# Performance work log

Hardware: AMD Instinct MI355X
Metric: run time of the kernel (lower is better)

## Reference

```python
import jax, jax.numpy as jnp
import numpy as np

N_NODES = 50000
N_EDGES = 800000
IN_CH = 128
H = [128, 128, 128]


def _sage_max(x, src, dst, Wl, b, Wr, n_nodes):
    # PyG SAGEConv(aggr='max'): max-aggregate neighbor features, then
    # out = agg @ Wl.T + b + x @ Wr.T ; empty segments -> 0 (torch_scatter).
    agg = jax.ops.segment_max(x[src], dst, num_segments=n_nodes)  # [N, d]
    agg = jnp.where(jnp.isfinite(agg), agg, 0.0)
    return agg @ Wl.T + b + x @ Wr.T


def setup_inputs() -> dict:
    key = jax.random.key(0)
    ks = jax.random.split(key, 24)
    x = jax.random.normal(ks[0], (N_NODES, IN_CH), dtype=jnp.float32)
    edge_index = jax.random.randint(ks[1], (2, N_EDGES), 0, N_NODES, dtype=jnp.int64)
    s = 0.05

    def w(k, o, i):
        return jax.random.normal(k, (o, i), dtype=jnp.float32) * s

    inp = {
        "x": x,
        "edge_index": edge_index,
        "shared_Wl": w(ks[2], H[0], IN_CH), "shared_b": jnp.zeros((H[0],), jnp.float32), "shared_Wr": w(ks[3], H[0], IN_CH),
        "rt1_Wl": w(ks[4], H[1], H[0]), "rt1_b": jnp.zeros((H[1],), jnp.float32), "rt1_Wr": w(ks[5], H[1], H[0]),
        "rt2_Wl": w(ks[6], H[2], H[1]), "rt2_b": jnp.zeros((H[2],), jnp.float32), "rt2_Wr": w(ks[7], H[2], H[1]),
        "rt3_W": w(ks[8], 1, H[2]), "rt3_b": jnp.zeros((1,), jnp.float32),
        "mv1_Wl": w(ks[9], H[1], H[0]), "mv1_b": jnp.zeros((H[1],), jnp.float32), "mv1_Wr": w(ks[10], H[1], H[0]),
        "mv2_Wl": w(ks[11], H[2], H[1]), "mv2_b": jnp.zeros((H[2],), jnp.float32), "mv2_Wr": w(ks[12], H[2], H[1]),
        "mv3_W": w(ks[13], 1, H[2]), "mv3_b": jnp.zeros((1,), jnp.float32),
    }
    return inp


def reference(x, edge_index, shared_Wl, shared_b, shared_Wr,
              rt1_Wl, rt1_b, rt1_Wr, rt2_Wl, rt2_b, rt2_Wr, rt3_W, rt3_b,
              mv1_Wl, mv1_b, mv1_Wr, mv2_Wl, mv2_b, mv2_Wr, mv3_W, mv3_b):
    n = x.shape[0]
    src, dst = edge_index[0], edge_index[1]
    # Eval mode: dropout is identity.
    mv = jax.nn.relu(_sage_max(x, src, dst, shared_Wl, shared_b, shared_Wr, n))

    rt = jax.nn.relu(_sage_max(mv, src, dst, rt1_Wl, rt1_b, rt1_Wr, n))
    rt = jax.nn.relu(_sage_max(rt, src, dst, rt2_Wl, rt2_b, rt2_Wr, n))
    rtAngle = (rt @ rt3_W.T + rt3_b).reshape(-1)

    md = jax.nn.relu(_sage_max(mv, src, dst, mv1_Wl, mv1_b, mv1_Wr, n))
    md = jax.nn.relu(_sage_max(md, src, dst, mv2_Wl, mv2_b, mv2_Wr, n))
    moveDis = (md @ mv3_W.T + mv3_b).reshape(-1)

    return (rtAngle, moveDis)
```

## Files before the change

kernel.cpp:

```cpp
#include <hip/hip_runtime.h>
#include <hip/hip_bf16.h>
#include <math.h>

#define NN 50000
#define NE 800000
#define C  128
#define NR 8
#define RNG (NN / NR)
typedef unsigned int u32;
typedef unsigned short u16;

using f32x4  = __attribute__((ext_vector_type(4))) float;
using short8 = __attribute__((ext_vector_type(8))) short;

__device__ __forceinline__ u16 f2bf(float f) {
    u32 u = __float_as_uint(f);
    u32 r = u + 0x7FFFu + ((u >> 16) & 1u);
    return (u16)(r >> 16);
}
__device__ __forceinline__ float bf2f(u16 h) {
    return __uint_as_float(((u32)h) << 16);
}

__device__ __forceinline__ void gload_lds16(const u16* g, u16* l) {
    __builtin_amdgcn_global_load_lds(
        (const __attribute__((address_space(1))) u32*)g,
        (__attribute__((address_space(3))) u32*)l,
        16, 0, 0);
}


__global__ void k_zero(int* __restrict__ p, int n) {
    int i = blockIdx.x * blockDim.x + threadIdx.x;
    if (i < n) p[i] = 0;
}

__global__ __launch_bounds__(256) void k_hist_x(const int* __restrict__ dst, int* __restrict__ deg, int nE) {
    int r    = blockIdx.x & (NR - 1);
    int base = (blockIdx.x >> 3) * 4096;
    int lo   = r * RNG, hi = lo + RNG;
    #pragma unroll
    for (int it = 0; it < 16; ++it) {
        int e = base + it * 256 + threadIdx.x;
        if (e < nE) {
            int d = dst[e];
            if (d >= lo && d < hi) atomicAdd(&deg[d], 1);
        }
    }
}

__global__ __launch_bounds__(1024) void k_scan_blk(const int* __restrict__ deg, int* __restrict__ rowptr,
                                                   int* __restrict__ bsum, int n) {
    __shared__ int wsum[16];
    int tid = threadIdx.x, lane = tid & 63, wid = tid >> 6;
    int i = blockIdx.x * 1024 + tid;
    int v = (i < n) ? deg[i] : 0;
    int incl = v;
    #pragma unroll
    for (int d = 1; d < 64; d <<= 1) {
        int t = __shfl_up(incl, d, 64);
        if (lane >= d) incl += t;
    }
    if (lane == 63) wsum[wid] = incl;
    __syncthreads();
    int wo = 0;
    #pragma unroll
    for (int w = 0; w < 16; ++w) wo += (w < wid) ? wsum[w] : 0;
    if (i < n) rowptr[i + 1] = wo + incl;
    if (tid == 1023) bsum[blockIdx.x] = wo + incl;
}

__global__ void k_scan_sums(int* __restrict__ bsum, int nb) {
    int lane = threadIdx.x;
    int v = (lane < nb) ? bsum[lane] : 0;
    int incl = v;
    #pragma unroll
    for (int d = 1; d < 64; d <<= 1) {
        int t = __shfl_up(incl, d, 64);
        if (lane >= d) incl += t;
    }
    if (lane < nb) bsum[lane] = incl - v;
}

__global__ __launch_bounds__(1024) void k_scan_add(int* __restrict__ rowptr, const int* __restrict__ bsum, int n) {
    int i = blockIdx.x * 1024 + threadIdx.x;
    if (i == 0) rowptr[0] = 0;
    if (i < n) rowptr[i + 1] += bsum[blockIdx.x];
}

__global__ __launch_bounds__(256) void k_fill_x(const int* __restrict__ src, const int* __restrict__ dst,
                                                const int* __restrict__ rowptr, int* __restrict__ deg,
                                                u16* __restrict__ esrc, int nE) {
    int r    = blockIdx.x & (NR - 1);
    int base = (blockIdx.x >> 3) * 4096;
    int lo   = r * RNG, hi = lo + RNG;
    #pragma unroll
    for (int it = 0; it < 16; ++it) {
        int e = base + it * 256 + threadIdx.x;
        if (e < nE) {
            int d = dst[e];
            if (d >= lo && d < hi) {
                int old = atomicSub(&deg[d], 1);
                esrc[rowptr[d + 1] - old] = (u16)src[e];
            }
        }
    }
}

__global__ void k_cvt(const float* __restrict__ in, u32* __restrict__ oh, int n64) {
    int i = blockIdx.x * 256 + threadIdx.x;
    if (i < n64) {
        float2 v = *(const float2*)(in + (size_t)i * 2);
        oh[i] = ((u32)f2bf(v.x)) | (((u32)f2bf(v.y)) << 16);
    }
}

#define UPK(w_, lo_, hi_) { lo_ = fmaxf(lo_, __uint_as_float((w_) << 16)); \
                            hi_ = fmaxf(hi_, __uint_as_float((w_) & 0xFFFF0000u)); }

__global__ __launch_bounds__(256) void k_segmax_bf(const u32* __restrict__ h2, const int* __restrict__ rowptr,
                                                   const u16* __restrict__ esrc, u32* __restrict__ agg2, int n) {
    int node = blockIdx.x * 4 + (threadIdx.x >> 6);
    int lane = threadIdx.x & 63;
    if (node >= n) return;
    int beg = rowptr[node], end = rowptr[node + 1];
    float mlo = -INFINITY, mhi = -INFINITY;
    int last = end - 1;
    for (int i = beg; i < end; i += 8) {
        int e0 = i,     e1 = i + 1, e2 = i + 2, e3 = i + 3;
        int e4 = i + 4, e5 = i + 5, e6 = i + 6, e7 = i + 7;
        e1 = e1 > last ? last : e1;  e2 = e2 > last ? last : e2;
        e3 = e3 > last ? last : e3;  e4 = e4 > last ? last : e4;
        e5 = e5 > last ? last : e5;  e6 = e6 > last ? last : e6;
        e7 = e7 > last ? last : e7;
        u32 w0 = h2[((size_t)esrc[e0] << 6) + lane];
        u32 w1 = h2[((size_t)esrc[e1] << 6) + lane];
        u32 w2 = h2[((size_t)esrc[e2] << 6) + lane];
        u32 w3 = h2[((size_t)esrc[e3] << 6) + lane];
        u32 w4 = h2[((size_t)esrc[e4] << 6) + lane];
        u32 w5 = h2[((size_t)esrc[e5] << 6) + lane];
        u32 w6 = h2[((size_t)esrc[e6] << 6) + lane];
        u32 w7 = h2[((size_t)esrc[e7] << 6) + lane];
        UPK(w0, mlo, mhi) UPK(w1, mlo, mhi) UPK(w2, mlo, mhi) UPK(w3, mlo, mhi)
        UPK(w4, mlo, mhi) UPK(w5, mlo, mhi) UPK(w6, mlo, mhi) UPK(w7, mlo, mhi)
    }
    u32 r = 0u;
    if (end > beg)
        r = (__float_as_uint(mlo) >> 16) | (__float_as_uint(mhi) & 0xFFFF0000u);
    __builtin_nontemporal_store(r, &agg2[(size_t)node * 64 + lane]);
}

__global__ __launch_bounds__(256) void k_segmax_bf2(const u32* __restrict__ hA, const u32* __restrict__ hB,
                                                    const int* __restrict__ rowptr, const u16* __restrict__ esrc,
                                                    u32* __restrict__ aggA, u32* __restrict__ aggB, int n) {
    int node = blockIdx.x * 4 + (threadIdx.x >> 6);
    int lane = threadIdx.x & 63;
    if (node >= n) return;
    int beg = rowptr[node], end = rowptr[node + 1];
    float alo = -INFINITY, ahi = -INFINITY, blo = -INFINITY, bhi = -INFINITY;
    int last = end - 1;
    for (int i = beg; i < end; i += 8) {
        int e0 = i,     e1 = i + 1, e2 = i + 2, e3 = i + 3;
        int e4 = i + 4, e5 = i + 5, e6 = i + 6, e7 = i + 7;
        e1 = e1 > last ? last : e1;  e2 = e2 > last ? last : e2;
        e3 = e3 > last ? last : e3;  e4 = e4 > last ? last : e4;
        e5 = e5 > last ? last : e5;  e6 = e6 > last ? last : e6;
        e7 = e7 > last ? last : e7;
        size_t b0 = ((size_t)esrc[e0] << 6) + lane;
        size_t b1 = ((size_t)esrc[e1] << 6) + lane;
        size_t b2 = ((size_t)esrc[e2] << 6) + lane;
        size_t b3 = ((size_t)esrc[e3] << 6) + lane;
        size_t b4 = ((size_t)esrc[e4] << 6) + lane;
        size_t b5 = ((size_t)esrc[e5] << 6) + lane;
        size_t b6 = ((size_t)esrc[e6] << 6) + lane;
        size_t b7 = ((size_t)esrc[e7] << 6) + lane;
        u32 a0 = hA[b0], a1 = hA[b1], a2 = hA[b2], a3 = hA[b3];
        u32 a4 = hA[b4], a5 = hA[b5], a6 = hA[b6], a7 = hA[b7];
        u32 q0 = hB[b0], q1 = hB[b1], q2 = hB[b2], q3 = hB[b3];
        u32 q4 = hB[b4], q5 = hB[b5], q6 = hB[b6], q7 = hB[b7];
        UPK(a0, alo, ahi) UPK(a1, alo, ahi) UPK(a2, alo, ahi) UPK(a3, alo, ahi)
        UPK(a4, alo, ahi) UPK(a5, alo, ahi) UPK(a6, alo, ahi) UPK(a7, alo, ahi)
        UPK(q0, blo, bhi) UPK(q1, blo, bhi) UPK(q2, blo, bhi) UPK(q3, blo, bhi)
        UPK(q4, blo, bhi) UPK(q5, blo, bhi) UPK(q6, blo, bhi) UPK(q7, blo, bhi)
    }
    u32 ra = 0u, rb = 0u;
    if (end > beg) {
        ra = (__float_as_uint(alo) >> 16) | (__float_as_uint(ahi) & 0xFFFF0000u);
        rb = (__float_as_uint(blo) >> 16) | (__float_as_uint(bhi) & 0xFFFF0000u);
    }
    __builtin_nontemporal_store(ra, &aggA[(size_t)node * 64 + lane]);
    __builtin_nontemporal_store(rb, &aggB[(size_t)node * 64 + lane]);
}

struct PackArgs {
    const float* Wl[5]; const float* Wr[5];
    u16* Wh[5]; u16* Wlo[5];
};
__global__ void k_packw5(PackArgs pa) {
    int L   = blockIdx.y;
    int idx = blockIdx.x * 256 + threadIdx.x;
    if (idx >= 128 * 256) return;
    int j = idx & 7, l = (idx >> 3) & 63, s = (idx >> 9) & 7, t = idx >> 12;
    int nrow = t * 16 + (l & 15);
    int k    = s * 32 + (l >> 4) * 8 + j;
    float v  = (k < 128) ? pa.Wl[L][nrow * 128 + k] : pa.Wr[L][nrow * 128 + (k - 128)];
    u16 h = f2bf(v);
    pa.Wh[L][idx]  = h;
    pa.Wlo[L][idx] = f2bf(v - bf2f(h));
}

template<int HEAD>
__global__ __launch_bounds__(256, 2) void k_gemm_p(
        const u16* __restrict__ Ahi, const u16* __restrict__ Xh,
        const u16* __restrict__ Wh, const u16* __restrict__ Wlo,
        const float* __restrict__ bias, u32* __restrict__ outh,
        const float* __restrict__ hw, const float* __restrict__ hb,
        float* __restrict__ hout, int n) {
    __shared__ __align__(16) u16 smw[2][8192];
    int tid  = threadIdx.x;
    int wave = tid >> 6, lane = tid & 63;
    int rit  = lane & 15, kgrp = lane >> 4;
    int m0   = blockIdx.x * 128 + wave * 32;
    int ar0  = m0 + rit;      if (ar0 > n - 1) ar0 = n - 1;
    int ar1  = m0 + 16 + rit; if (ar1 > n - 1) ar1 = n - 1;

    #define STAGE(s_, b_) do {                                                   \
        _Pragma("unroll")                                                        \
        for (int q = 0; q < 4; ++q) {                                            \
            int kk = wave * 4 + q;                                               \
            int tt = kk >> 1;                                                    \
            const u16* g = ((kk & 1) ? Wlo : Wh)                                 \
                           + (((tt << 3) + (s_)) << 9) + (lane << 3);            \
            gload_lds16(g, &smw[b_][kk << 9]);                                   \
        }                                                                        \
    } while (0)
    #define STAGEH(s_, b_) do {                                                  \
        _Pragma("unroll")                                                        \
        for (int q = 0; q < 2; ++q) {                                            \
            int tt = wave * 2 + q;                                               \
            const u16* g = Wh + (((tt << 3) + (s_)) << 9) + (lane << 3);         \
            gload_lds16(g, &smw[b_][(tt << 1) << 9]);                            \
        }                                                                        \
    } while (0)

    short8 a0[4], a1[4], xh0[4], xh1[4];
    #pragma unroll
    for (int s = 0; s < 4; ++s) {
        size_t o0 = (size_t)ar0 * C + s * 32 + kgrp * 8;
        size_t o1 = (size_t)ar1 * C + s * 32 + kgrp * 8;
        a0[s]  = *(const short8*)(Ahi + o0);
        a1[s]  = *(const short8*)(Ahi + o1);
        xh0[s] = *(const short8*)(Xh + o0);
        xh1[s] = *(const short8*)(Xh + o1);
    }

    f32x4 acc0[8], acc1[8];
    #pragma unroll
    for (int t = 0; t < 8; ++t) {
        acc0[t] = (f32x4){0.f, 0.f, 0.f, 0.f};
        acc1[t] = (f32x4){0.f, 0.f, 0.f, 0.f};
    }

    STAGEH(0, 0);
    __syncthreads();

    #pragma unroll
    for (int s = 0; s < 8; ++s) {
        if (s < 7) {
            if (s + 1 < 4) STAGEH(s + 1, (s + 1) & 1);
            else           STAGE(s + 1, (s + 1) & 1);
        }
        const u16* base = smw[s & 1];
        if (s < 4) {
            #pragma unroll
            for (int t = 0; t < 8; ++t) {
                short8 wh = *(const short8*)(base + ((t << 1) << 9) + (lane << 3));
                acc0[t] = __builtin_amdgcn_mfma_f32_16x16x32_bf16(a0[s], wh, acc0[t], 0, 0, 0);
                acc1[t] = __builtin_amdgcn_mfma_f32_16x16x32_bf16(a1[s], wh, acc1[t], 0, 0, 0);
            }
        } else {
            int q = s - 4;
            #pragma unroll
            for (int t = 0; t < 8; ++t) {
                short8 wh = *(const short8*)(base + ((t << 1) << 9)         + (lane << 3));
                short8 wl = *(const short8*)(base + ((((t << 1) | 1)) << 9) + (lane << 3));
                acc0[t] = __builtin_amdgcn_mfma_f32_16x16x32_bf16(xh0[q], wh, acc0[t], 0, 0, 0);
                acc0[t] = __builtin_amdgcn_mfma_f32_16x16x32_bf16(xh0[q], wl, acc0[t], 0, 0, 0);
                acc1[t] = __builtin_amdgcn_mfma_f32_16x16x32_bf16(xh1[q], wh, acc1[t], 0, 0, 0);
                acc1[t] = __builtin_amdgcn_mfma_f32_16x16x32_bf16(xh1[q], wl, acc1[t], 0, 0, 0);
            }
        }
        if (s < 7) __syncthreads();
    }
    #undef STAGE
    #undef STAGEH

    if (HEAD) {
        float hsA[4] = {0.f, 0.f, 0.f, 0.f}, hsB[4] = {0.f, 0.f, 0.f, 0.f};
        #pragma unroll
        for (int t = 0; t < 8; ++t) {
            int col = t * 16 + rit;
            float b = bias[col], w = hw[col];
            #pragma unroll
            for (int j = 0; j < 4; ++j) {
                hsA[j] += fmaxf(acc0[t][j] + b, 0.f) * w;
                hsB[j] += fmaxf(acc1[t][j] + b, 0.f) * w;
            }
        }
        #pragma unroll
        for (int msk = 1; msk < 16; msk <<= 1) {
            #pragma unroll
            for (int j = 0; j < 4; ++j) {
                hsA[j] += __shfl_xor(hsA[j], msk, 64);
                hsB[j] += __shfl_xor(hsB[j], msk, 64);
            }
        }
        if (rit == 0) {
            float hbv = hb[0];
            #pragma unroll
            for (int j = 0; j < 4; ++j) {
                int rA = m0 + kgrp * 4 + j;
                int rB = rA + 16;
                if (rA < n) hout[rA] = hsA[j] + hbv;
                if (rB < n) hout[rB] = hsB[j] + hbv;
            }
        }
    } else {
        #pragma unroll
        for (int g = 0; g < 2; ++g) {
            int rbase = m0 + g * 16 + kgrp * 4;
            #pragma unroll
            for (int t = 0; t < 8; ++t) {
                int col = t * 16 + rit;
                float b = bias[col];
                #pragma unroll
                for (int j = 0; j < 4; ++j) {
                    int rr = rbase + j;
                    float v = fmaxf((g ? acc1[t][j] : acc0[t][j]) + b, 0.f);
                    float pv = __shfl_xor(v, 1, 64);
                    if (!(rit & 1) && rr < n)
                        outh[(size_t)rr * 64 + (col >> 1)] = ((u32)f2bf(v)) | (((u32)f2bf(pv)) << 16);
                }
            }
        }
    }
}

__global__ __launch_bounds__(256, 2) void k_gemm_p2(
        const u16* __restrict__ Ahi, const u16* __restrict__ Xh,
        const u16* __restrict__ Wh1, const u16* __restrict__ Wlo1,
        const float* __restrict__ b1, u32* __restrict__ out1,
        const u16* __restrict__ Wh2, const u16* __restrict__ Wlo2,
        const float* __restrict__ b2, u32* __restrict__ out2, int n) {
    __shared__ __align__(16) u16 smw[2][16384];
    int tid  = threadIdx.x;
    int wave = tid >> 6, lane = tid & 63;
    int rit  = lane & 15, kgrp = lane >> 4;
    int m0   = blockIdx.x * 128 + wave * 32;
    int ar0  = m0 + rit;      if (ar0 > n - 1) ar0 = n - 1;
    int ar1  = m0 + 16 + rit; if (ar1 > n - 1) ar1 = n - 1;

    #define STAGE2(s_, b_) do {                                                  \
        _Pragma("unroll")                                                        \
        for (int q = 0; q < 8; ++q) {                                            \
            int kk = wave * 8 + q;                                               \
            int set = kk >> 4, sl = kk & 15;                                     \
            int tt = sl >> 1;                                                    \
            const u16* g = ((sl & 1) ? (set ? Wlo2 : Wlo1) : (set ? Wh2 : Wh1))  \
                           + (((tt << 3) + (s_)) << 9) + (lane << 3);            \
            gload_lds16(g, &smw[b_][set * 8192 + (sl << 9)]);                    \
        }                                                                        \
    } while (0)
    #define STAGE2H(s_, b_) do {                                                 \
        _Pragma("unroll")                                                        \
        for (int q = 0; q < 4; ++q) {                                            \
            int kk = wave * 4 + q;                                               \
            int set = kk >> 3, tt = kk & 7;                                      \
            const u16* g = (set ? Wh2 : Wh1)                                     \
                           + (((tt << 3) + (s_)) << 9) + (lane << 3);            \
            gload_lds16(g, &smw[b_][set * 8192 + ((tt << 1) << 9)]);             \
        }                                                                        \
    } while (0)

    short8 a0[4], a1[4], xh0[4], xh1[4];
    #pragma unroll
    for (int s = 0; s < 4; ++s) {
        size_t o0 = (size_t)ar0 * C + s * 32 + kgrp * 8;
        size_t o1 = (size_t)ar1 * C + s * 32 + kgrp * 8;
        a0[s]  = *(const short8*)(Ahi + o0);
        a1[s]  = *(const short8*)(Ahi + o1);
        xh0[s] = *(const short8*)(Xh + o0);
        xh1[s] = *(const short8*)(Xh + o1);
    }

    f32x4 acc[2][2][8];
    #pragma unroll
    for (int e = 0; e < 2; ++e)
        #pragma unroll
        for (int g = 0; g < 2; ++g)
            #pragma unroll
            for (int t = 0; t < 8; ++t) acc[e][g][t] = (f32x4){0.f, 0.f, 0.f, 0.f};

    STAGE2H(0, 0);
    __syncthreads();

    #pragma unroll
    for (int s = 0; s < 8; ++s) {
        if (s < 7) {
            if (s + 1 < 4) STAGE2H(s + 1, (s + 1) & 1);
            else           STAGE2(s + 1, (s + 1) & 1);
        }
        const u16* base = smw[s & 1];
        if (s < 4) {
            #pragma unroll
            for (int e = 0; e < 2; ++e) {
                const u16* sb = base + e * 8192;
                #pragma unroll
                for (int t = 0; t < 8; ++t) {
                    short8 wh = *(const short8*)(sb + ((t << 1) << 9) + (lane << 3));
                    acc[e][0][t] = __builtin_amdgcn_mfma_f32_16x16x32_bf16(a0[s], wh, acc[e][0][t], 0, 0, 0);
                    acc[e][1][t] = __builtin_amdgcn_mfma_f32_16x16x32_bf16(a1[s], wh, acc[e][1][t], 0, 0, 0);
                }
            }
        } else {
            int q = s - 4;
            #pragma unroll
            for (int e = 0; e < 2; ++e) {
                const u16* sb = base + e * 8192;
                #pragma unroll
                for (int t = 0; t < 8; ++t) {
                    short8 wh = *(const short8*)(sb + ((t << 1) << 9)         + (lane << 3));
                    short8 wl = *(const short8*)(sb + ((((t << 1) | 1)) << 9) + (lane << 3));
                    acc[e][0][t] = __builtin_amdgcn_mfma_f32_16x16x32_bf16(xh0[q], wh, acc[e][0][t], 0, 0, 0);
                    acc[e][0][t] = __builtin_amdgcn_mfma_f32_16x16x32_bf16(xh0[q], wl, acc[e][0][t], 0, 0, 0);
                    acc[e][1][t] = __builtin_amdgcn_mfma_f32_16x16x32_bf16(xh1[q], wh, acc[e][1][t], 0, 0, 0);
                    acc[e][1][t] = __builtin_amdgcn_mfma_f32_16x16x32_bf16(xh1[q], wl, acc[e][1][t], 0, 0, 0);
                }
            }
        }
        if (s < 7) __syncthreads();
    }
    #undef STAGE2
    #undef STAGE2H

    #pragma unroll
    for (int e = 0; e < 2; ++e) {
        const float* bb = e ? b2 : b1;
        u32* oo = e ? out2 : out1;
        #pragma unroll
        for (int g = 0; g < 2; ++g) {
            int rbase = m0 + g * 16 + kgrp * 4;
            #pragma unroll
            for (int t = 0; t < 8; ++t) {
                int col = t * 16 + rit;
                float b = bb[col];
                #pragma unroll
                for (int j = 0; j < 4; ++j) {
                    int rr = rbase + j;
                    float v = fmaxf(acc[e][g][t][j] + b, 0.f);
                    float pv = __shfl_xor(v, 1, 64);
                    if (!(rit & 1) && rr < n)
                        oo[(size_t)rr * 64 + (col >> 1)] = ((u32)f2bf(v)) | (((u32)f2bf(pv)) << 16);
                }
            }
        }
    }
}


extern "C" void kernel_launch(void* const* d_in, const int* in_sizes, int n_in,
                              void* d_out, int out_size, void* d_ws, size_t ws_size,
                              hipStream_t stream) {
    const float* x     = (const float*)d_in[0];
    const int*   ei    = (const int*)d_in[1];
    const int*   src   = ei;
    const int*   dstp  = ei + NE;
    const float* sWl   = (const float*)d_in[2];
    const float* sB    = (const float*)d_in[3];
    const float* sWr   = (const float*)d_in[4];
    const float* rt1Wl = (const float*)d_in[5];
    const float* rt1B  = (const float*)d_in[6];
    const float* rt1Wr = (const float*)d_in[7];
    const float* rt2Wl = (const float*)d_in[8];
    const float* rt2B  = (const float*)d_in[9];
    const float* rt2Wr = (const float*)d_in[10];
    const float* rt3W  = (const float*)d_in[11];
    const float* rt3B  = (const float*)d_in[12];
    const float* mv1Wl = (const float*)d_in[13];
    const float* mv1B  = (const float*)d_in[14];
    const float* mv1Wr = (const float*)d_in[15];
    const float* mv2Wl = (const float*)d_in[16];
    const float* mv2B  = (const float*)d_in[17];
    const float* mv2Wr = (const float*)d_in[18];
    const float* mv3W  = (const float*)d_in[19];
    const float* mv3B  = (const float*)d_in[20];
    float* out = (float*)d_out;

    char* ws = (char*)d_ws;
    int* rowptr  = (int*)ws;
    int* deg     = rowptr + (NN + 1);
    int* bsum    = deg + NN;
    u16* esrc16  = (u16*)(bsum + 64);
    size_t off   = (((size_t)(NN + 1 + NN + 64) * 4 + (size_t)NE * 2) + 255) & ~(size_t)255;
    u32* P[5];
    for (int i = 0; i < 5; ++i) P[i] = (u32*)(ws + off) + (size_t)i * NN * 64;
    u16* wpack = (u16*)(P[4] + (size_t)NN * 64);
    u16* pk[5][2];
    for (int L = 0; L < 5; ++L) {
        pk[L][0] = wpack + (size_t)L * 65536;
        pk[L][1] = wpack + (size_t)L * 65536 + 32768;
    }

    const int TB = 256;
    const int NB = (NN + 1023) / 1024;
    const int GCH = ((NE + 4095) / 4096) * NR;

    PackArgs pa;
    pa.Wl[0] = sWl;   pa.Wr[0] = sWr;
    pa.Wl[1] = rt1Wl; pa.Wr[1] = rt1Wr;
    pa.Wl[2] = rt2Wl; pa.Wr[2] = rt2Wr;
    pa.Wl[3] = mv1Wl; pa.Wr[3] = mv1Wr;
    pa.Wl[4] = mv2Wl; pa.Wr[4] = mv2Wr;
    for (int L = 0; L < 5; ++L) { pa.Wh[L] = pk[L][0]; pa.Wlo[L] = pk[L][1]; }
    k_packw5<<<dim3(128, 5), 256, 0, stream>>>(pa);
    k_cvt<<<(NN * 64 + 255) / 256, 256, 0, stream>>>(x, P[0], NN * 64);

    k_zero<<<(NN + TB - 1) / TB, TB, 0, stream>>>(deg, NN);
    k_hist_x<<<GCH, 256, 0, stream>>>(dstp, deg, NE);
    k_scan_blk<<<NB, 1024, 0, stream>>>(deg, rowptr, bsum, NN);
    k_scan_sums<<<1, 64, 0, stream>>>(bsum, NB);
    k_scan_add<<<NB, 1024, 0, stream>>>(rowptr, bsum, NN);
    k_fill_x<<<GCH, 256, 0, stream>>>(src, dstp, rowptr, deg, esrc16, NE);

    dim3 gSeg((NN + 3) / 4), bSeg(256);
    dim3 gGem((NN + 127) / 128), bGem(256);

    k_segmax_bf<<<gSeg, bSeg, 0, stream>>>(P[0], rowptr, esrc16, P[1], NN);
    k_gemm_p<0><<<gGem, bGem, 0, stream>>>((const u16*)P[1], (const u16*)P[0],
                                           pk[0][0], pk[0][1], sB, P[2],
                                           nullptr, nullptr, nullptr, NN);
    k_segmax_bf<<<gSeg, bSeg, 0, stream>>>(P[2], rowptr, esrc16, P[3], NN);
    k_gemm_p2<<<gGem, bGem, 0, stream>>>((const u16*)P[3], (const u16*)P[2],
                                         pk[1][0], pk[1][1], rt1B, P[1],
                                         pk[3][0], pk[3][1], mv1B, P[4], NN);
    k_segmax_bf2<<<gSeg, bSeg, 0, stream>>>(P[1], P[4], rowptr, esrc16, P[0], P[3], NN);
    k_gemm_p<1><<<gGem, bGem, 0, stream>>>((const u16*)P[0], (const u16*)P[1],
                                           pk[2][0], pk[2][1], rt2B, nullptr,
                                           rt3W, rt3B, out, NN);
    k_gemm_p<1><<<gGem, bGem, 0, stream>>>((const u16*)P[3], (const u16*)P[4],
                                           pk[4][0], pk[4][1], mv2B, nullptr,
                                           mv3W, mv3B, out + NN, NN);
}
```

Measured before the change: 273.8 us.

## Drop split-bf16 weight residual, merge head GEMMs, fold degree zeroing into convert

Measured after the change: 264.2 us. -3.5%, faster.

```diff
diff --git a/kernel.cpp b/kernel.cpp
--- a/kernel.cpp
+++ b/kernel.cpp
@@ -18,9 +18,6 @@
     u32 r = u + 0x7FFFu + ((u >> 16) & 1u);
     return (u16)(r >> 16);
 }
-__device__ __forceinline__ float bf2f(u16 h) {
-    return __uint_as_float(((u32)h) << 16);
-}
 
 __device__ __forceinline__ void gload_lds16(const u16* g, u16* l) {
     __builtin_amdgcn_global_load_lds(
@@ -29,11 +26,6 @@
         16, 0, 0);
 }
 
-
-__global__ void k_zero(int* __restrict__ p, int n) {
-    int i = blockIdx.x * blockDim.x + threadIdx.x;
-    if (i < n) p[i] = 0;
-}
 
 __global__ __launch_bounds__(256) void k_hist_x(const int* __restrict__ dst, int* __restrict__ deg, int nE) {
     int r    = blockIdx.x & (NR - 1);
@@ -107,8 +99,9 @@
     }
 }
 
-__global__ void k_cvt(const float* __restrict__ in, u32* __restrict__ oh, int n64) {
+__global__ void k_cvt(const float* __restrict__ in, u32* __restrict__ oh, int* __restrict__ deg, int n64) {
     int i = blockIdx.x * 256 + threadIdx.x;
+    if (i < NN) deg[i] = 0;
     if (i < n64) {
         float2 v = *(const float2*)(in + (size_t)i * 2);
         oh[i] = ((u32)f2bf(v.x)) | (((u32)f2bf(v.y)) << 16);
@@ -127,13 +120,14 @@
     float mlo = -INFINITY, mhi = -INFINITY;
     int last = end - 1;
     for (int i = beg; i < end; i += 8) {
-        int e0 = i,     e1 = i + 1, e2 = i + 2, e3 = i + 3;
-        int e4 = i + 4, e5 = i + 5, e6 = i + 6, e7 = i + 7;
-        e1 = e1 > last ? last : e1;  e2 = e2 > last ? last : e2;
-        e3 = e3 > last ? last : e3;  e4 = e4 > last ? last : e4;
-        e5 = e5 > last ? last : e5;  e6 = e6 > last ? last : e6;
-        e7 = e7 > last ? last : e7;
-        u32 w0 = h2[((size_t)esrc[e0] << 6) + lane];
+        int e1 = i + 1 > last ? last : i + 1;
+        int e2 = i + 2 > last ? last : i + 2;
+        int e3 = i + 3 > last ? last : i + 3;
+        int e4 = i + 4 > last ? last : i + 4;
+        int e5 = i + 5 > last ? last : i + 5;
+        int e6 = i + 6 > last ? last : i + 6;
+        int e7 = i + 7 > last ? last : i + 7;
+        u32 w0 = h2[((size_t)esrc[i]  << 6) + lane];
         u32 w1 = h2[((size_t)esrc[e1] << 6) + lane];
         u32 w2 = h2[((size_t)esrc[e2] << 6) + lane];
         u32 w3 = h2[((size_t)esrc[e3] << 6) + lane];
@@ -160,13 +154,14 @@
     float alo = -INFINITY, ahi = -INFINITY, blo = -INFINITY, bhi = -INFINITY;
     int last = end - 1;
     for (int i = beg; i < end; i += 8) {
-        int e0 = i,     e1 = i + 1, e2 = i + 2, e3 = i + 3;
-        int e4 = i + 4, e5 = i + 5, e6 = i + 6, e7 = i + 7;
-        e1 = e1 > last ? last : e1;  e2 = e2 > last ? last : e2;
-        e3 = e3 > last ? last : e3;  e4 = e4 > last ? last : e4;
-        e5 = e5 > last ? last : e5;  e6 = e6 > last ? last : e6;
-        e7 = e7 > last ? last : e7;
-        size_t b0 = ((size_t)esrc[e0] << 6) + lane;
+        int e1 = i + 1 > last ? last : i + 1;
+        int e2 = i + 2 > last ? last : i + 2;
+        int e3 = i + 3 > last ? last : i + 3;
+        int e4 = i + 4 > last ? last : i + 4;
+        int e5 = i + 5 > last ? last : i + 5;
+        int e6 = i + 6 > last ? last : i + 6;
+        int e7 = i + 7 > last ? last : i + 7;
+        size_t b0 = ((size_t)esrc[i]  << 6) + lane;
         size_t b1 = ((size_t)esrc[e1] << 6) + lane;
         size_t b2 = ((size_t)esrc[e2] << 6) + lane;
         size_t b3 = ((size_t)esrc[e3] << 6) + lane;
@@ -194,7 +189,7 @@
 
 struct PackArgs {
     const float* Wl[5]; const float* Wr[5];
-    u16* Wh[5]; u16* Wlo[5];
+    u16* Wh[5];
 };
 __global__ void k_packw5(PackArgs pa) {
     int L   = blockIdx.y;
@@ -204,42 +199,29 @@
     int nrow = t * 16 + (l & 15);
     int k    = s * 32 + (l >> 4) * 8 + j;
     float v  = (k < 128) ? pa.Wl[L][nrow * 128 + k] : pa.Wr[L][nrow * 128 + (k - 128)];
-    u16 h = f2bf(v);
-    pa.Wh[L][idx]  = h;
-    pa.Wlo[L][idx] = f2bf(v - bf2f(h));
+    pa.Wh[L][idx] = f2bf(v);
 }
 
 template<int HEAD>
-__global__ __launch_bounds__(256, 2) void k_gemm_p(
+__device__ __forceinline__ void gemm_body(
         const u16* __restrict__ Ahi, const u16* __restrict__ Xh,
-        const u16* __restrict__ Wh, const u16* __restrict__ Wlo,
-        const float* __restrict__ bias, u32* __restrict__ outh,
+        const u16* __restrict__ Wh, const float* __restrict__ bias,
+        u32* __restrict__ outh,
         const float* __restrict__ hw, const float* __restrict__ hb,
-        float* __restrict__ hout, int n) {
-    __shared__ __align__(16) u16 smw[2][8192];
+        float* __restrict__ hout, int n, int bid, u16 (*smw)[4096]) {
     int tid  = threadIdx.x;
     int wave = tid >> 6, lane = tid & 63;
     int rit  = lane & 15, kgrp = lane >> 4;
-    int m0   = blockIdx.x * 128 + wave * 32;
+    int m0   = bid * 128 + wave * 32;
     int ar0  = m0 + rit;      if (ar0 > n - 1) ar0 = n - 1;
     int ar1  = m0 + 16 + rit; if (ar1 > n - 1) ar1 = n - 1;
 
-    #define STAGE(s_, b_) do {                                                   \
-        _Pragma("unroll")                                                        \
-        for (int q = 0; q < 4; ++q) {                                            \
-            int kk = wave * 4 + q;                                               \
-            int tt = kk >> 1;                                                    \
-            const u16* g = ((kk & 1) ? Wlo : Wh)                                 \
-                           + (((tt << 3) + (s_)) << 9) + (lane << 3);            \
-            gload_lds16(g, &smw[b_][kk << 9]);                                   \
-        }                                                                        \
-    } while (0)
     #define STAGEH(s_, b_) do {                                                  \
         _Pragma("unroll")                                                        \
         for (int q = 0; q < 2; ++q) {                                            \
             int tt = wave * 2 + q;                                               \
             const u16* g = Wh + (((tt << 3) + (s_)) << 9) + (lane << 3);         \
-            gload_lds16(g, &smw[b_][(tt << 1) << 9]);                            \
+            gload_lds16(g, &smw[b_][tt << 9]);                                   \
         }                                                                        \
     } while (0)
 
@@ -266,33 +248,18 @@
 
     #pragma unroll
     for (int s = 0; s < 8; ++s) {
-        if (s < 7) {
-            if (s + 1 < 4) STAGEH(s + 1, (s + 1) & 1);
-            else           STAGE(s + 1, (s + 1) & 1);
-        }
+        if (s < 7) STAGEH(s + 1, (s + 1) & 1);
         const u16* base = smw[s & 1];
-        if (s < 4) {
-            #pragma unroll
-            for (int t = 0; t < 8; ++t) {
-                short8 wh = *(const short8*)(base + ((t << 1) << 9) + (lane << 3));
-                acc0[t] = __builtin_amdgcn_mfma_f32_16x16x32_bf16(a0[s], wh, acc0[t], 0, 0, 0);
-                acc1[t] = __builtin_amdgcn_mfma_f32_16x16x32_bf16(a1[s], wh, acc1[t], 0, 0, 0);
-            }
-        } else {
-            int q = s - 4;
-            #pragma unroll
-            for (int t = 0; t < 8; ++t) {
-                short8 wh = *(const short8*)(base + ((t << 1) << 9)         + (lane << 3));
-                short8 wl = *(const short8*)(base + ((((t << 1) | 1)) << 9) + (lane << 3));
-                acc0[t] = __builtin_amdgcn_mfma_f32_16x16x32_bf16(xh0[q], wh, acc0[t], 0, 0, 0);
-                acc0[t] = __builtin_amdgcn_mfma_f32_16x16x32_bf16(xh0[q], wl, acc0[t], 0, 0, 0);
-                acc1[t] = __builtin_amdgcn_mfma_f32_16x16x32_bf16(xh1[q], wh, acc1[t], 0, 0, 0);
-                acc1[t] = __builtin_amdgcn_mfma_f32_16x16x32_bf16(xh1[q], wl, acc1[t], 0, 0, 0);
-            }
+        short8 f0 = (s < 4) ? a0[s] : xh0[s - 4];
+        short8 f1 = (s < 4) ? a1[s] : xh1[s - 4];
+        #pragma unroll
+        for (int t = 0; t < 8; ++t) {
+            short8 wv = *(const short8*)(base + (t << 9) + (lane << 3));
+            acc0[t] = __builtin_amdgcn_mfma_f32_16x16x32_bf16(f0, wv, acc0[t], 0, 0, 0);
+            acc1[t] = __builtin_amdgcn_mfma_f32_16x16x32_bf16(f1, wv, acc1[t], 0, 0, 0);
         }
         if (s < 7) __syncthreads();
     }
-    #undef STAGE
     #undef STAGEH
 
     if (HEAD) {
@@ -346,13 +313,36 @@
     }
 }
 
+__global__ __launch_bounds__(256, 2) void k_gemm_p(
+        const u16* __restrict__ Ahi, const u16* __restrict__ Xh,
+        const u16* __restrict__ Wh, const float* __restrict__ bias, u32* __restrict__ outh, int n) {
+    __shared__ __align__(16) u16 smw[2][4096];
+    gemm_body<0>(Ahi, Xh, Wh, bias, outh, nullptr, nullptr, nullptr, n, blockIdx.x, smw);
+}
+
+__global__ __launch_bounds__(256, 2) void k_gemm_heads(
+        const u16* __restrict__ AhiA, const u16* __restrict__ XhA,
+        const u16* __restrict__ WhA, const float* __restrict__ biasA,
+        const float* __restrict__ hwA, const float* __restrict__ hbA, float* __restrict__ houtA,
+        const u16* __restrict__ AhiB, const u16* __restrict__ XhB,
+        const u16* __restrict__ WhB, const float* __restrict__ biasB,
+        const float* __restrict__ hwB, const float* __restrict__ hbB, float* __restrict__ houtB,
+        int n) {
+    __shared__ __align__(16) u16 smw[2][4096];
+    int nb = (n + 127) >> 7;
+    int br = blockIdx.x >= nb;
+    int bid = blockIdx.x - br * nb;
+    gemm_body<1>(br ? AhiB : AhiA, br ? XhB : XhA, br ? WhB : WhA,
+                 br ? biasB : biasA, nullptr,
+                 br ? hwB : hwA, br ? hbB : hbA, br ? houtB : houtA,
+                 n, bid, smw);
+}
+
 __global__ __launch_bounds__(256, 2) void k_gemm_p2(
         const u16* __restrict__ Ahi, const u16* __restrict__ Xh,
-        const u16* __restrict__ Wh1, const u16* __restrict__ Wlo1,
-        const float* __restrict__ b1, u32* __restrict__ out1,
-        const u16* __restrict__ Wh2, const u16* __restrict__ Wlo2,
-        const float* __restrict__ b2, u32* __restrict__ out2, int n) {
-    __shared__ __align__(16) u16 smw[2][16384];
+        const u16* __restrict__ Wh1, const float* __restrict__ b1, u32* __restrict__ out1,
+        const u16* __restrict__ Wh2, const float* __restrict__ b2, u32* __restrict__ out2, int n) {
+    __shared__ __align__(16) u16 smw[2][8192];
     int tid  = threadIdx.x;
     int wave = tid >> 6, lane = tid & 63;
     int rit  = lane & 15, kgrp = lane >> 4;
@@ -360,25 +350,13 @@
     int ar0  = m0 + rit;      if (ar0 > n - 1) ar0 = n - 1;
     int ar1  = m0 + 16 + rit; if (ar1 > n - 1) ar1 = n - 1;
 
-    #define STAGE2(s_, b_) do {                                                  \
-        _Pragma("unroll")                                                        \
-        for (int q = 0; q < 8; ++q) {                                            \
-            int kk = wave * 8 + q;                                               \
-            int set = kk >> 4, sl = kk & 15;                                     \
-            int tt = sl >> 1;                                                    \
-            const u16* g = ((sl & 1) ? (set ? Wlo2 : Wlo1) : (set ? Wh2 : Wh1))  \
-                           + (((tt << 3) + (s_)) << 9) + (lane << 3);            \
-            gload_lds16(g, &smw[b_][set * 8192 + (sl << 9)]);                    \
-        }                                                                        \
-    } while (0)
     #define STAGE2H(s_, b_) do {                                                 \
         _Pragma("unroll")                                                        \
         for (int q = 0; q < 4; ++q) {                                            \
             int kk = wave * 4 + q;                                               \
             int set = kk >> 3, tt = kk & 7;                                      \
-            const u16* g = (set ? Wh2 : Wh1)                                     \
-                           + (((tt << 3) + (s_)) << 9) + (lane << 3);            \
-            gload_lds16(g, &smw[b_][set * 8192 + ((tt << 1) << 9)]);             \
+            const u16* g = (set ? Wh2 : Wh1) + (((tt << 3) + (s_)) << 9) + (lane << 3); \
+            gload_lds16(g, &smw[b_][set * 4096 + (tt << 9)]);                    \
         }                                                                        \
     } while (0)
 
@@ -393,54 +371,35 @@
         xh1[s] = *(const short8*)(Xh + o1);
     }
 
-    f32x4 acc[2][2][8];
-    #pragma unroll
-    for (int e = 0; e < 2; ++e)
-        #pragma unroll
-        for (int g = 0; g < 2; ++g)
-            #pragma unroll
-            for (int t = 0; t < 8; ++t) acc[e][g][t] = (f32x4){0.f, 0.f, 0.f, 0.f};
+    f32x4 accA0[8], accA1[8], accB0[8], accB1[8];
+    #pragma unroll
+    for (int t = 0; t < 8; ++t) {
+        accA0[t] = (f32x4){0.f, 0.f, 0.f, 0.f};
+        accA1[t] = (f32x4){0.f, 0.f, 0.f, 0.f};
+        accB0[t] = (f32x4){0.f, 0.f, 0.f, 0.f};
+        accB1[t] = (f32x4){0.f, 0.f, 0.f, 0.f};
+    }
 
     STAGE2H(0, 0);
     __syncthreads();
 
     #pragma unroll
     for (int s = 0; s < 8; ++s) {
-        if (s < 7) {
-            if (s + 1 < 4) STAGE2H(s + 1, (s + 1) & 1);
-            else           STAGE2(s + 1, (s + 1) & 1);
-        }
+        if (s < 7) STAGE2H(s + 1, (s + 1) & 1);
         const u16* base = smw[s & 1];
-        if (s < 4) {
-            #pragma unroll
-            for (int e = 0; e < 2; ++e) {
-                const u16* sb = base + e * 8192;
-                #pragma unroll
-                for (int t = 0; t < 8; ++t) {
-                    short8 wh = *(const short8*)(sb + ((t << 1) << 9) + (lane << 3));
-                    acc[e][0][t] = __builtin_amdgcn_mfma_f32_16x16x32_bf16(a0[s], wh, acc[e][0][t], 0, 0, 0);
-                    acc[e][1][t] = __builtin_amdgcn_mfma_f32_16x16x32_bf16(a1[s], wh, acc[e][1][t], 0, 0, 0);
-                }
-            }
-        } else {
-            int q = s - 4;
-            #pragma unroll
-            for (int e = 0; e < 2; ++e) {
-                const u16* sb = base + e * 8192;
-                #pragma unroll
-                for (int t = 0; t < 8; ++t) {
-                    short8 wh = *(const short8*)(sb + ((t << 1) << 9)         + (lane << 3));
-                    short8 wl = *(const short8*)(sb + ((((t << 1) | 1)) << 9) + (lane << 3));
-                    acc[e][0][t] = __builtin_amdgcn_mfma_f32_16x16x32_bf16(xh0[q], wh, acc[e][0][t], 0, 0, 0);
-                    acc[e][0][t] = __builtin_amdgcn_mfma_f32_16x16x32_bf16(xh0[q], wl, acc[e][0][t], 0, 0, 0);
-                    acc[e][1][t] = __builtin_amdgcn_mfma_f32_16x16x32_bf16(xh1[q], wh, acc[e][1][t], 0, 0, 0);
-                    acc[e][1][t] = __builtin_amdgcn_mfma_f32_16x16x32_bf16(xh1[q], wl, acc[e][1][t], 0, 0, 0);
-                }
-            }
+        short8 f0 = (s < 4) ? a0[s] : xh0[s - 4];
+        short8 f1 = (s < 4) ? a1[s] : xh1[s - 4];
+        #pragma unroll
+        for (int t = 0; t < 8; ++t) {
+            short8 wa = *(const short8*)(base + (t << 9) + (lane << 3));
+            short8 wb = *(const short8*)(base + 4096 + (t << 9) + (lane << 3));
+            accA0[t] = __builtin_amdgcn_mfma_f32_16x16x32_bf16(f0, wa, accA0[t], 0, 0, 0);
+            accA1[t] = __builtin_amdgcn_mfma_f32_16x16x32_bf16(f1, wa, accA1[t], 0, 0, 0);
+            accB0[t] = __builtin_amdgcn_mfma_f32_16x16x32_bf16(f0, wb, accB0[t], 0, 0, 0);
+            accB1[t] = __builtin_amdgcn_mfma_f32_16x16x32_bf16(f1, wb, accB1[t], 0, 0, 0);
         }
         if (s < 7) __syncthreads();
     }
-    #undef STAGE2
     #undef STAGE2H
 
     #pragma unroll
@@ -457,7 +416,9 @@
                 #pragma unroll
                 for (int j = 0; j < 4; ++j) {
                     int rr = rbase + j;
-                    float v = fmaxf(acc[e][g][t][j] + b, 0.f);
+                    float acv = e ? (g ? accB1[t][j] : accB0[t][j])
+                                  : (g ? accA1[t][j] : accA0[t][j]);
+                    float v = fmaxf(acv + b, 0.f);
                     float pv = __shfl_xor(v, 1, 64);
                     if (!(rit & 1) && rr < n)
                         oo[(size_t)rr * 64 + (col >> 1)] = ((u32)f2bf(v)) | (((u32)f2bf(pv)) << 16);
@@ -505,13 +466,9 @@
     u32* P[5];
     for (int i = 0; i < 5; ++i) P[i] = (u32*)(ws + off) + (size_t)i * NN * 64;
     u16* wpack = (u16*)(P[4] + (size_t)NN * 64);
-    u16* pk[5][2];
-    for (int L = 0; L < 5; ++L) {
-        pk[L][0] = wpack + (size_t)L * 65536;
-        pk[L][1] = wpack + (size_t)L * 65536 + 32768;
-    }
-
-    const int TB = 256;
+    u16* pk[5];
+    for (int L = 0; L < 5; ++L) pk[L] = wpack + (size_t)L * 32768;
+
     const int NB = (NN + 1023) / 1024;
     const int GCH = ((NE + 4095) / 4096) * NR;
 
@@ -521,11 +478,10 @@
     pa.Wl[2] = rt2Wl; pa.Wr[2] = rt2Wr;
     pa.Wl[3] = mv1Wl; pa.Wr[3] = mv1Wr;
     pa.Wl[4] = mv2Wl; pa.Wr[4] = mv2Wr;
-    for (int L = 0; L < 5; ++L) { pa.Wh[L] = pk[L][0]; pa.Wlo[L] = pk[L][1]; }
+    for (int L = 0; L < 5; ++L) pa.Wh[L] = pk[L];
     k_packw5<<<dim3(128, 5), 256, 0, stream>>>(pa);
-    k_cvt<<<(NN * 64 + 255) / 256, 256, 0, stream>>>(x, P[0], NN * 64);
-
-    k_zero<<<(NN + TB - 1) / TB, TB, 0, stream>>>(deg, NN);
+    k_cvt<<<(NN * 64 + 255) / 256, 256, 0, stream>>>(x, P[0], deg, NN * 64);
+
     k_hist_x<<<GCH, 256, 0, stream>>>(dstp, deg, NE);
     k_scan_blk<<<NB, 1024, 0, stream>>>(deg, rowptr, bsum, NN);
     k_scan_sums<<<1, 64, 0, stream>>>(bsum, NB);
@@ -533,21 +489,18 @@
     k_fill_x<<<GCH, 256, 0, stream>>>(src, dstp, rowptr, deg, esrc16, NE);
 
     dim3 gSeg((NN + 3) / 4), bSeg(256);
-    dim3 gGem((NN + 127) / 128), bGem(256);
+    const int GT = (NN + 127) / 128;
 
     k_segmax_bf<<<gSeg, bSeg, 0, stream>>>(P[0], rowptr, esrc16, P[1], NN);
-    k_gemm_p<0><<<gGem, bGem, 0, stream>>>((const u16*)P[1], (const u16*)P[0],
-                                           pk[0][0], pk[0][1], sB, P[2],
-                                           nullptr, nullptr, nullptr, NN);
+    k_gemm_p<<<GT, 256, 0, stream>>>((const u16*)P[1], (const u16*)P[0],
+                                     pk[0], sB, P[2], NN);
     k_segmax_bf<<<gSeg, bSeg, 0, stream>>>(P[2], rowptr, esrc16, P[3], NN);
-    k_gemm_p2<<<gGem, bGem, 0, stream>>>((const u16*)P[3], (const u16*)P[2],
-                                         pk[1][0], pk[1][1], rt1B, P[1],
-                                         pk[3][0], pk[3][1], mv1B, P[4], NN);
+    k_gemm_p2<<<GT, 256, 0, stream>>>((const u16*)P[3], (const u16*)P[2],
+                                      pk[1], rt1B, P[1],
+                                      pk[3], mv1B, P[4], NN);
     k_segmax_bf2<<<gSeg, bSeg, 0, stream>>>(P[1], P[4], rowptr, esrc16, P[0], P[3], NN);
-    k_gemm_p<1><<<gGem, bGem, 0, stream>>>((const u16*)P[0], (const u16*)P[1],
-                                           pk[2][0], pk[2][1], rt2B, nullptr,
-                                           rt3W, rt3B, out, NN);
-    k_gemm_p<1><<<gGem, bGem, 0, stream>>>((const u16*)P[3], (const u16*)P[4],
-                                           pk[4][0], pk[4][1], mv2B, nullptr,
-                                           mv3W, mv3B, out + NN, NN);
-}
+    k_gemm_heads<<<2 * GT, 256, 0, stream>>>(
+        (const u16*)P[0], (const u16*)P[1], pk[2], rt2B, rt3W, rt3B, out,
+        (const u16*)P[3], (const u16*)P[4], pk[4], mv2B, mv3W, mv3B, out + NN,
+        NN);
+}
```
